# Performance work log

Measured on AMD Instinct MI355X. Metric: run time of the kernel, lower is better.

Reference implementation:

```python
import jax, jax.numpy as jnp
import numpy as np

BANDS, D_MODEL, NCLASS = 200, 256, 17
EXPAND, D_STATE, D_CONV, HEADDIM = 2, 128, 4, 64
D_INNER = EXPAND * D_MODEL            # 512
NHEADS = D_INNER // HEADDIM           # 8
D_IN_PROJ = 2 * D_INNER + 2 * D_STATE + NHEADS  # 1288 (ngroups=1)
CHUNK = 256


def _segsum(a):
    # a: (..., Q) -> (..., Q, Q); out[i,j] = sum_{k=j+1..i} a[k] (i>=j), else -inf
    q = a.shape[-1]
    cs = jnp.cumsum(a, axis=-1)
    d = cs[..., :, None] - cs[..., None, :]
    mask = jnp.tril(jnp.ones((q, q), dtype=bool))
    return jnp.where(mask, d, -jnp.inf)


def _ssd(Xd, Adt, B, C, Q):
    # Chunked SSD (exact selective-scan). Xd=(b,l,h,p) is x*dt, Adt=(b,l,h) is A*dt, B,C=(b,l,n)
    b, l, h, p = Xd.shape
    n = B.shape[-1]
    c = l // Q
    Xc = Xd.reshape(b, c, Q, h, p)
    Bc = B.reshape(b, c, Q, n)
    Cc = C.reshape(b, c, Q, n)
    Ac = Adt.reshape(b, c, Q, h).transpose(0, 3, 1, 2)      # (b,h,c,Q)
    Acs = jnp.cumsum(Ac, axis=-1)
    Lm = jnp.exp(_segsum(Ac))                                # (b,h,c,Q,Q) lower-tri decay
    Yd = jnp.einsum('bcqn,bckn,bhcqk,bckhp->bcqhp', Cc, Bc, Lm, Xc)
    decay_states = jnp.exp(Acs[..., -1:] - Acs)              # (b,h,c,Q)
    states = jnp.einsum('bcqn,bhcq,bcqhp->bchpn', Bc, decay_states, Xc)
    chunk_decay = jnp.exp(Acs[..., -1])                      # (b,h,c)
    def step(carry, inp):
        s, d = inp
        return carry * d[..., None, None] + s, carry
    _, prev = jax.lax.scan(step, jnp.zeros((b, h, p, n), Xd.dtype),
                           (states.transpose(1, 0, 2, 3, 4), chunk_decay.transpose(2, 0, 1)))
    prev = prev.transpose(1, 0, 2, 3, 4)                     # (b,c,h,p,n) state entering each chunk
    Yo = jnp.einsum('bcqn,bchpn,bhcq->bcqhp', Cc, prev, jnp.exp(Acs))
    return (Yd + Yo).reshape(b, l, h, p)


def setup_inputs() -> dict:
    ks = jax.random.split(jax.random.key(0), 8)
    b, l = 16, 1024
    dt0 = jnp.exp(jax.random.uniform(ks[1], (NHEADS,), minval=np.log(1e-3), maxval=np.log(0.1)))
    return {
        'x': jax.random.normal(ks[0], (b, l, BANDS), jnp.float32),
        'w_inp': jax.random.normal(ks[2], (BANDS, D_MODEL)) * 0.05,
        'b_inp': jnp.zeros((D_MODEL,)),
        'w_in': jax.random.normal(ks[3], (D_MODEL, D_IN_PROJ)) * 0.05,
        'conv_w': jax.random.normal(ks[4], (D_CONV, D_INNER + 2 * D_STATE)) * 0.2,
        'conv_b': jnp.zeros((D_INNER + 2 * D_STATE,)),
        'dt_bias': jnp.log(jnp.expm1(dt0)),                 # inverse softplus
        'A_log': jnp.log(jnp.arange(1, NHEADS + 1, dtype=jnp.float32)),
        'D': jnp.ones((NHEADS,)),
        'rms_w': jnp.ones((D_INNER,)),
        'w_out': jax.random.normal(ks[5], (D_INNER, D_MODEL)) * 0.04,
        'ln_g': jnp.ones((D_MODEL,)),
        'ln_b': jnp.zeros((D_MODEL,)),
        'w_cls': jax.random.normal(ks[6], (D_MODEL, NCLASS)) * 0.06,
        'b_cls': jnp.zeros((NCLASS,)),
    }


def reference(x, w_inp, b_inp, w_in, conv_w, conv_b, dt_bias, A_log, D,
              rms_w, w_out, ln_g, ln_b, w_cls, b_cls):
    b, l, _ = x.shape
    u = x @ w_inp + b_inp                                    # input_proj: (b,l,d_model)
    zxbcdt = u @ w_in                                        # (b,l,1288)
    z, xBC, dt = jnp.split(zxbcdt, [D_INNER, 2 * D_INNER + 2 * D_STATE], axis=-1)
    dt = jax.nn.softplus(dt + dt_bias)                       # (b,l,nheads)
    # causal depthwise conv1d + SiLU
    xBC = jax.lax.conv_general_dilated(
        xBC, conv_w[:, None, :], (1,), [(D_CONV - 1, 0)],
        dimension_numbers=('NWC', 'WIO', 'NWC'),
        feature_group_count=D_INNER + 2 * D_STATE) + conv_b
    xBC = jax.nn.silu(xBC)
    xh, B, C = jnp.split(xBC, [D_INNER, D_INNER + D_STATE], axis=-1)
    xh = xh.reshape(b, l, NHEADS, HEADDIM)
    A = -jnp.exp(A_log)                                      # (nheads,)
    y = _ssd(xh * dt[..., None], dt * A, B, C, CHUNK)        # (b,l,h,p)
    y = y + xh * D[None, None, :, None]                      # D skip
    y = y.reshape(b, l, D_INNER)
    # gated RMSNorm (norm_before_gate=False): rmsnorm(y * silu(z)) * w
    y = y * jax.nn.silu(z)
    y = y * jax.lax.rsqrt(jnp.mean(y * y, axis=-1, keepdims=True) + 1e-5) * rms_w
    y = y @ w_out                                            # out_proj (no bias)
    # classifier: LayerNorm -> Dropout(eval=identity) -> Linear
    mu = jnp.mean(y, axis=-1, keepdims=True)
    var = jnp.mean((y - mu) ** 2, axis=-1, keepdims=True)
    y = (y - mu) * jax.lax.rsqrt(var + 1e-5) * ln_g + ln_b
    return y @ w_cls + b_cls
```

## Files before the change

kernel.cpp:

```cpp
#include <hip/hip_runtime.h>
#include <math.h>

#define ROWS   16384L
#define LSEQ   1024
#define NB     16
#define DM     256
#define DPROJ  1288
#define ZXW    1280
#define XBCW   768
#define DIN    512
#define DSTATE 128
#define NH     8
#define HD     64
#define QLEN   256
#define NCHUNK 4
#define NCLS   17

typedef __attribute__((ext_vector_type(8))) short s16x8;
typedef __attribute__((ext_vector_type(8))) unsigned short u16x8;
typedef __attribute__((ext_vector_type(4))) float f32x4;

#define GLOAD_LDS16(gsrc, ldst) \
  __builtin_amdgcn_global_load_lds((const __attribute__((address_space(1))) void*)(gsrc), \
      (__attribute__((address_space(3))) void*)(ldst), 16, 0, 0)

constexpr long O_GBF  = 0;
constexpr long O_ZX   = O_GBF + ROWS*DM;
constexpr long O_XBC  = O_ZX  + ROWS*DPROJ;
constexpr long O_DT   = O_XBC + ROWS*XBCW;
constexpr long O_ACS  = O_DT  + ROWS*NH;
constexpr long O_Y    = O_ACS + 131072;
constexpr long O_ST   = O_Y   + ROWS*DIN;
constexpr long O_Y2   = O_ST  + 4194304;
constexpr long O_XBF  = O_XBC;
constexpr long O_BBF  = O_XBC + 4200000;
constexpr long O_CBF  = O_XBC + 5300000;
constexpr long O_BT   = O_XBC + 6400000;
constexpr long O_YBF  = O_Y;
constexpr long O_XPBF = O_Y + 4300000;
constexpr long O_WCT  = O_Y + 6200000;
constexpr long O_WOUTT= O_Y + 6400000;
constexpr long O_WDT  = O_Y + 6500000;
constexpr long O_WCLST= O_Y + 6530000;
constexpr long O_WINT = O_Y + 6600000;
constexpr long O_WIPE = O_Y + 6800000;

__device__ inline unsigned short f2bf(float f) {
  union { float f; unsigned u; } v; v.f = f;
  unsigned r = v.u + 0x7FFFu + ((v.u >> 16) & 1u);
  return (unsigned short)(r >> 16);
}
__device__ inline float bf2f(unsigned short s) {
  union { unsigned u; float f; } v; v.u = ((unsigned)s) << 16; return v.f;
}

__device__ inline void xcd_swizzle(int gx, int& bx, int& by) {
  int nwg = gx * (int)gridDim.y;
  int lid = (int)blockIdx.y * gx + (int)blockIdx.x;
  int q = nwg >> 3, r = nwg & 7;
  int xcd = lid & 7, idx = lid >> 3;
  int base = xcd < r ? xcd * (q + 1) : r * (q + 1) + (xcd - r) * q;
  int w = base + idx;
  bx = w % gx; by = w / gx;
}

__global__ __launch_bounds__(256) void prep_misc(
    const float* __restrict__ x, unsigned short* __restrict__ xp,
    const float* __restrict__ w_in, unsigned short* __restrict__ w_inT,
    const float* __restrict__ wout, unsigned short* __restrict__ woutT,
    const float* __restrict__ w_inp, const float* __restrict__ b_inp,
    unsigned short* __restrict__ we,
    float* __restrict__ Wdt, float* __restrict__ bdt,
    const float* __restrict__ wcls, float* __restrict__ wclsT)
{
  int bid = blockIdx.x;
  int tid = threadIdx.x;
  if (bid < 3584) {
    long idx = (long)bid * 256 + tid;
    int q = (int)(idx % 56);
    long row = idx / 56;
    ushort4 o = {0, 0, 0, 0};
    if (q < 50) {
      float4 v = *(const float4*)&x[row * 200 + q * 4];
      o.x = f2bf(v.x); o.y = f2bf(v.y); o.z = f2bf(v.z); o.w = f2bf(v.w);
    } else if (q == 50) {
      o.x = 0x3F80;
    }
    *(ushort4*)&xp[row * 224 + q * 4] = o;
  } else if (bid < 4872) {
    long i = (long)(bid - 3584) * 256 + tid;
    int k = (int)(i & 255);
    long n = i >> 8;
    w_inT[i] = f2bf(w_in[(long)k * DPROJ + n]);
  } else if (bid < 5384) {
    long i = (long)(bid - 4872) * 256 + tid;
    int k = (int)(i & 511);
    long n = i >> 9;
    woutT[i] = f2bf(wout[(long)k * DM + n]);
  } else if (bid < 5608) {
    int i = (bid - 5384) * 256 + tid;
    int k = i >> 8, j = i & 255;
    float v = 0.f;
    if (k < 200)       v = w_inp[(long)k * 256 + j];
    else if (k == 200) v = b_inp[j];
    we[i] = f2bf(v);
  } else if (bid < 5659) {
    int k = (bid - 5608) * 4 + (tid >> 6);
    if (k > 200) return;
    int lane = tid & 63;
    int j0 = lane * 4;
    float4 xv = (k < 200) ? *(const float4*)&w_inp[(long)k * 256 + j0]
                          : *(const float4*)&b_inp[j0];
    float a0 = 0.f, a1 = 0.f, a2 = 0.f, a3 = 0.f, a4 = 0.f, a5 = 0.f, a6 = 0.f, a7 = 0.f;
    float xd[4] = {xv.x, xv.y, xv.z, xv.w};
#pragma unroll
    for (int d = 0; d < 4; ++d) {
      const float* wr = &w_in[(long)(j0 + d) * DPROJ + 1280];
      float4 wa = *(const float4*)wr;
      float4 wb = *(const float4*)(wr + 4);
      a0 = fmaf(xd[d], wa.x, a0); a1 = fmaf(xd[d], wa.y, a1);
      a2 = fmaf(xd[d], wa.z, a2); a3 = fmaf(xd[d], wa.w, a3);
      a4 = fmaf(xd[d], wb.x, a4); a5 = fmaf(xd[d], wb.y, a5);
      a6 = fmaf(xd[d], wb.z, a6); a7 = fmaf(xd[d], wb.w, a7);
    }
#pragma unroll
    for (int off = 32; off; off >>= 1) {
      a0 += __shfl_xor(a0, off); a1 += __shfl_xor(a1, off);
      a2 += __shfl_xor(a2, off); a3 += __shfl_xor(a3, off);
      a4 += __shfl_xor(a4, off); a5 += __shfl_xor(a5, off);
      a6 += __shfl_xor(a6, off); a7 += __shfl_xor(a7, off);
    }
    float o = a0;
    if (lane == 1) o = a1; if (lane == 2) o = a2; if (lane == 3) o = a3;
    if (lane == 4) o = a4; if (lane == 5) o = a5; if (lane == 6) o = a6;
    if (lane == 7) o = a7;
    if (lane < 8) {
      if (k < 200) Wdt[k * 8 + lane] = o;
      else         bdt[lane] = o;
    }
  } else {
    int i = (bid - 5659) * 256 + tid;
    if (i < NCLS * 256) {
      int j = i >> 8, k = i & 255;
      wclsT[i] = wcls[(long)k * NCLS + j];
    }
  }
}

__global__ __launch_bounds__(256) void gemm_bf16(
    const unsigned short* __restrict__ A, const unsigned short* __restrict__ BT,
    float* __restrict__ C, unsigned short* __restrict__ Cb,
    const float* __restrict__ bias, int M, int N, int K)
{
  int bx, by;
  xcd_swizzle(gridDim.x, bx, by);
  __shared__ __align__(16) unsigned short As[128 * 32];
  __shared__ __align__(16) unsigned short Bs[128 * 32];
  const int tid = threadIdx.x;
  const int m0 = by * 128, n0 = bx * 128;
  const int lane = tid & 63, wv = tid >> 6;
  const int wr = (wv >> 1) * 64, wc = (wv & 1) * 64;
  f32x4 acc[4][4];
#pragma unroll
  for (int i = 0; i < 4; ++i)
#pragma unroll
    for (int j = 0; j < 4; ++j) acc[i][j] = (f32x4){0.f, 0.f, 0.f, 0.f};

  for (int k0 = 0; k0 < K; k0 += 32) {
    __syncthreads();
#pragma unroll
    for (int s = 0; s < 2; ++s) {
      int idx = (tid + 256 * s) * 8;
      int r = idx >> 5, kk = idx & 31;
      GLOAD_LDS16(&A[(long)(m0 + r) * K + k0 + kk], &As[idx]);
    }
#pragma unroll
    for (int s = 0; s < 2; ++s) {
      int idx = (tid + 256 * s) * 8;
      int n = idx >> 5, kk = idx & 31;
      int srcn = (n0 + n < N) ? (n0 + n) : 0;
      GLOAD_LDS16(&BT[(long)srcn * K + k0 + kk], &Bs[idx]);
    }
    __syncthreads();
    s16x8 af[4], bf[4];
#pragma unroll
    for (int i = 0; i < 4; ++i)
      af[i] = *(const s16x8*)&As[(wr + i * 16 + (lane & 15)) * 32 + (lane >> 4) * 8];
#pragma unroll
    for (int j = 0; j < 4; ++j)
      bf[j] = *(const s16x8*)&Bs[(wc + j * 16 + (lane & 15)) * 32 + (lane >> 4) * 8];
    __builtin_amdgcn_s_setprio(1);
#pragma unroll
    for (int i = 0; i < 4; ++i)
#pragma unroll
      for (int j = 0; j < 4; ++j)
        acc[i][j] = __builtin_amdgcn_mfma_f32_16x16x32_bf16(af[i], bf[j], acc[i][j], 0, 0, 0);
    __builtin_amdgcn_s_setprio(0);
  }
  const int cr = (lane >> 4) * 4, cc = lane & 15;
#pragma unroll
  for (int i = 0; i < 4; ++i)
#pragma unroll
    for (int j = 0; j < 4; ++j) {
      int col = n0 + wc + j * 16 + cc;
      if (col < N) {
        long rowb = (long)(m0 + wr + i * 16 + cr);
        float bv = bias ? bias[col] : 0.f;
#pragma unroll
        for (int r = 0; r < 4; ++r) {
          float v = acc[i][j][r] + bv;
          if (C)  C[(rowb + r) * N + col] = v;
          if (Cb) Cb[(rowb + r) * (long)N + col] = f2bf(v);
        }
      }
    }
}

__global__ __launch_bounds__(256) void trans_g(
    const unsigned short* __restrict__ Bbf, unsigned short* __restrict__ BbfT,
    const unsigned short* __restrict__ Cbf, unsigned short* __restrict__ Gbf)
{
  const int bid = blockIdx.x;
  const int tid = threadIdx.x;
  if (bid < 128) {
    __shared__ unsigned short T[128][130];
    int bc = bid >> 1, kh = bid & 1;
    long rowbase = (long)(bc >> 2) * LSEQ + (bc & 3) * QLEN + kh * 128;
    for (int e = tid; e < 128 * 128; e += 256) {
      int r = e >> 7, n = e & 127;
      T[r][n] = Bbf[(rowbase + r) * 128 + n];
    }
    __syncthreads();
    for (int e = tid; e < 128 * 128; e += 256) {
      int n = e >> 7, k = e & 127;
      BbfT[((long)bc * 128 + n) * 256 + kh * 128 + k] = T[k][n];
    }
    return;
  }
  if (bid >= 320) {
    int bc = bid - 320;
    unsigned short* Gout = Gbf + (long)bc * 65536;
    s16x8 z = {};
    for (int e = tid; e < 128 * 16; e += 256) {
      int r = e >> 4, seg = e & 15;
      *(s16x8*)&Gout[(long)r * 256 + 128 + seg * 8] = z;
    }
    return;
  }
  int bid2 = bid - 128;
  int t = bid2 % 3, bc = bid2 / 3;
  int m0 = (t == 0) ? 0 : 128;
  int n0 = (t == 2) ? 128 : 0;
  unsigned short* Gout = Gbf + (long)bc * 65536;
  long rowbase = (long)(bc >> 2) * LSEQ + (bc & 3) * QLEN;
  const unsigned short* A  = Cbf + rowbase * 128;
  const unsigned short* BT = Bbf + rowbase * 128;
  __shared__ __align__(16) unsigned short As[128 * 32];
  __shared__ __align__(16) unsigned short Bs[128 * 32];
  const int lane = tid & 63, wv = tid >> 6;
  const int wr = (wv >> 1) * 64, wc = (wv & 1) * 64;
  f32x4 acc[4][4];
#pragma unroll
  for (int i = 0; i < 4; ++i)
#pragma unroll
    for (int j = 0; j < 4; ++j) acc[i][j] = (f32x4){0.f, 0.f, 0.f, 0.f};
  for (int k0 = 0; k0 < 128; k0 += 32) {
    __syncthreads();
#pragma unroll
    for (int s = 0; s < 2; ++s) {
      int idx = (tid + 256 * s) * 8;
      int r = idx >> 5, kk = idx & 31;
      GLOAD_LDS16(&A[(long)(m0 + r) * 128 + k0 + kk], &As[idx]);
      GLOAD_LDS16(&BT[(long)(n0 + r) * 128 + k0 + kk], &Bs[idx]);
    }
    __syncthreads();
    s16x8 af[4], bf[4];
#pragma unroll
    for (int i = 0; i < 4; ++i)
      af[i] = *(const s16x8*)&As[(wr + i * 16 + (lane & 15)) * 32 + (lane >> 4) * 8];
#pragma unroll
    for (int j = 0; j < 4; ++j)
      bf[j] = *(const s16x8*)&Bs[(wc + j * 16 + (lane & 15)) * 32 + (lane >> 4) * 8];
    __builtin_amdgcn_s_setprio(1);
#pragma unroll
    for (int i = 0; i < 4; ++i)
#pragma unroll
      for (int j = 0; j < 4; ++j)
        acc[i][j] = __builtin_amdgcn_mfma_f32_16x16x32_bf16(af[i], bf[j], acc[i][j], 0, 0, 0);
    __builtin_amdgcn_s_setprio(0);
  }
  const int cr = (lane >> 4) * 4, cc = lane & 15;
#pragma unroll
  for (int i = 0; i < 4; ++i)
#pragma unroll
    for (int j = 0; j < 4; ++j) {
      int col = n0 + wc + j * 16 + cc;
      int qb = m0 + wr + i * 16 + cr;
#pragma unroll
      for (int r = 0; r < 4; ++r)
        Gout[(long)(qb + r) * 256 + col] = (col <= qb + r) ? f2bf(acc[i][j][r]) : (unsigned short)0;
    }
}

__global__ __launch_bounds__(256) void conv_silu5(
    const unsigned short* __restrict__ zxb, const float* __restrict__ cw,
    const float* __restrict__ cb,
    unsigned short* __restrict__ Xbf, unsigned short* __restrict__ Bbf,
    unsigned short* __restrict__ Cbf)
{
  long idx = (long)blockIdx.x * 256 + threadIdx.x;
  if (idx >= (ROWS / 4) * 96) return;
  int co = (int)(idx % 96);
  long tmp = idx / 96;
  int tq = (int)(tmp & 255);
  int b = (int)(tmp >> 8);
  int ch = co * 8;
  long row0 = (long)b * LSEQ + tq * 4;
  u16x8 zv[7];
#pragma unroll
  for (int j = 0; j < 7; ++j) {
    if (j >= 3 || tq > 0)
      zv[j] = *(const u16x8*)&zxb[(row0 + j - 3) * ZXW + 512 + ch];
    else
      zv[j] = (u16x8){0, 0, 0, 0, 0, 0, 0, 0};
  }
  float cwv[4][8], cbv[8];
  {
    float4 b0 = *(const float4*)&cb[ch];
    float4 b1 = *(const float4*)&cb[ch + 4];
    cbv[0] = b0.x; cbv[1] = b0.y; cbv[2] = b0.z; cbv[3] = b0.w;
    cbv[4] = b1.x; cbv[5] = b1.y; cbv[6] = b1.z; cbv[7] = b1.w;
  }
#pragma unroll
  for (int w = 0; w < 4; ++w) {
    float4 c0 = *(const float4*)&cw[w * XBCW + ch];
    float4 c1 = *(const float4*)&cw[w * XBCW + ch + 4];
    cwv[w][0] = c0.x; cwv[w][1] = c0.y; cwv[w][2] = c0.z; cwv[w][3] = c0.w;
    cwv[w][4] = c1.x; cwv[w][5] = c1.y; cwv[w][6] = c1.z; cwv[w][7] = c1.w;
  }
#pragma unroll
  for (int i = 0; i < 4; ++i) {
    float a[8];
#pragma unroll
    for (int k = 0; k < 8; ++k) a[k] = cbv[k];
#pragma unroll
    for (int w = 0; w < 4; ++w) {
#pragma unroll
      for (int k = 0; k < 8; ++k)
        a[k] = fmaf(bf2f(zv[i + w][k]), cwv[w][k], a[k]);
    }
    u16x8 o;
#pragma unroll
    for (int k = 0; k < 8; ++k)
      o[k] = f2bf(a[k] / (1.f + __expf(-a[k])));
    long row = row0 + i;
    if (ch < 512)      *(u16x8*)&Xbf[row * DIN + ch] = o;
    else if (ch < 640) *(u16x8*)&Bbf[row * 128 + ch - 512] = o;
    else               *(u16x8*)&Cbf[row * 128 + ch - 640] = o;
  }
}

__global__ __launch_bounds__(256) void dt_logits(
    const float* __restrict__ x, const float* __restrict__ Wdt,
    const float* __restrict__ bdt, const float* __restrict__ dtb,
    float* __restrict__ dtsp)
{
  __shared__ float xs[32][201];
  __shared__ float wdt_s[1600];
  long row0 = (long)blockIdx.x * 32;
  int tid = threadIdx.x;
#pragma unroll
  for (int s = 0; s < 25; ++s) {
    int e = tid + s * 256;
    int r = e / 200, c = e % 200;
    xs[r][c] = x[(row0 + r) * 200 + c];
  }
#pragma unroll
  for (int s = 0; s < 7; ++s) {
    int e = tid + s * 256;
    if (e < 1600) wdt_s[e] = Wdt[e];
  }
  __syncthreads();
  int r = tid >> 3, h = tid & 7;
  float acc = dtb[h] + bdt[h];
  for (int i = 0; i < 200; ++i)
    acc = fmaf(xs[r][i], wdt_s[i * 8 + h], acc);
  float sp = (acc > 20.f) ? acc : log1pf(__expf(acc));
  dtsp[(row0 + r) * NH + h] = sp;
}

__global__ __launch_bounds__(256) void dt_cumsum4(
    const float* __restrict__ dtsp, const float* __restrict__ alog,
    float* __restrict__ acs)
{
  int g = ((int)blockIdx.x * 256 + (int)threadIdx.x) >> 6;
  int lane = threadIdx.x & 63;
  int c = g & 3, h = (g >> 2) & 7, b = g >> 5;
  float Ah = -__expf(alog[h]);
  long rowbase = (long)b * LSEQ + c * QLEN;
  long abase = (((long)b * NH + h) * NCHUNK + c) * QLEN;
  float v[4];
#pragma unroll
  for (int j = 0; j < 4; ++j)
    v[j] = dtsp[(rowbase + lane * 4 + j) * NH + h] * Ah;
  v[1] += v[0]; v[2] += v[1]; v[3] += v[2];
  float tot = v[3];
  float run = tot;
#pragma unroll
  for (int d = 1; d < 64; d <<= 1) {
    float t = __shfl_up(run, d);
    if (lane >= d) run += t;
  }
  float excl = run - tot;
#pragma unroll
  for (int j = 0; j < 4; ++j) acs[abase + lane * 4 + j] = excl + v[j];
}

__global__ __launch_bounds__(256) void yd_states7(
    const unsigned short* __restrict__ Xbf, const float* __restrict__ dtsp,
    const float* __restrict__ acs, const unsigned short* __restrict__ Gbf,
    const unsigned short* __restrict__ BbfT,
    unsigned short* __restrict__ ybf, unsigned short* __restrict__ st)
{
  int bid = blockIdx.x;
  int xcd = bid & 7, i0 = bid >> 3;
  int bc = xcd * 8 + (i0 >> 4);
  int rem = i0 & 15, h = rem >> 1, half = rem & 1;
  int c = bc & 3, b = bc >> 2;
  int bch = bc * 8 + h;

  __shared__ __align__(16) unsigned short XdT[64][264];
  __shared__ float AcsS[256], E1f[256], E2f[256], dts[256];

  const int tid = threadIdx.x;
  const int lane = tid & 63, wv = tid >> 6;
  const bool ydw = wv < 2;
  const int qb = half == 0 ? (wv == 0 ? 0 : 3) : (wv == 0 ? 1 : 2);
  const int q0 = qb * 64;
  const int n0w = half * 64 + (wv - 2) * 32;
  long rowbase = (long)b * LSEQ + c * QLEN;
  const unsigned short* Gb  = Gbf + (long)bc * 65536;
  const unsigned short* BTg = BbfT + (long)bc * 32768;

  AcsS[tid] = acs[(((long)b * NH + h) * NCHUNK + c) * QLEN + tid];
  dts[tid]  = dtsp[(rowbase + tid) * NH + h];
  __syncthreads();
  E1f[tid] = __expf(AcsS[tid] - AcsS[tid | 63]);
  E2f[tid] = __expf(AcsS[tid | 63] - AcsS[tid]);
  float rs_[4];
  rs_[0] = 1.f;
#pragma unroll
  for (int kt = 1; kt < 4; ++kt) rs_[kt] = __expf(AcsS[kt * 64 + 63] - AcsS[kt * 64 - 1]);
  __syncthreads();
  {
    int kb = wv * 64;
#pragma unroll
    for (int s = 0; s < 16; ++s) {
      int k4 = kb + s * 4;
      ushort4 pk;
      unsigned short* pp = (unsigned short*)&pk;
#pragma unroll
      for (int j = 0; j < 4; ++j) {
        int k = k4 + j;
        float v = bf2f(Xbf[(rowbase + k) * DIN + h * HD + lane]) * dts[k] * E2f[k];
        pp[j] = f2bf(v);
      }
      *(ushort4*)&XdT[lane][k4] = pk;
    }
  }
  __syncthreads();

  f32x4 accY[4][4], accS[4][2];
#pragma unroll
  for (int i = 0; i < 4; ++i)
#pragma unroll
    for (int j = 0; j < 4; ++j) accY[i][j] = (f32x4){0.f, 0.f, 0.f, 0.f};
#pragma unroll
  for (int i = 0; i < 4; ++i)
#pragma unroll
    for (int j = 0; j < 2; ++j) accS[i][j] = (f32x4){0.f, 0.f, 0.f, 0.f};

  for (int kt = 0; kt < 4; ++kt) {
    int qlo = kt * 64;
    if (ydw) {
      if (qb >= kt) {
        if (kt)
#pragma unroll
          for (int i = 0; i < 4; ++i)
#pragma unroll
            for (int j = 0; j < 4; ++j) accY[i][j] *= rs_[kt];
#pragma unroll
        for (int ks = 0; ks < 2; ++ks) {
          s16x8 bfr[4];
#pragma unroll
          for (int j = 0; j < 4; ++j)
            bfr[j] = *(const s16x8*)&XdT[j * 16 + (lane & 15)][qlo + ks * 32 + (lane >> 4) * 8];
          __builtin_amdgcn_s_setprio(1);
#pragma unroll
          for (int i = 0; i < 4; ++i) {
            s16x8 a = *(const s16x8*)&Gb[(long)(q0 + i * 16 + (lane & 15)) * 256 + qlo + ks * 32 + (lane >> 4) * 8];
#pragma unroll
            for (int j = 0; j < 4; ++j)
              accY[i][j] = __builtin_amdgcn_mfma_f32_16x16x32_bf16(a, bfr[j], accY[i][j], 0, 0, 0);
          }
          __builtin_amdgcn_s_setprio(0);
        }
      }
    } else {
      if (kt)
#pragma unroll
        for (int i = 0; i < 4; ++i)
#pragma unroll
          for (int j = 0; j < 2; ++j) accS[i][j] *= rs_[kt];
#pragma unroll
      for (int ks = 0; ks < 2; ++ks) {
        s16x8 afx[4];
#pragma unroll
        for (int i = 0; i < 4; ++i)
          afx[i] = *(const s16x8*)&XdT[i * 16 + (lane & 15)][qlo + ks * 32 + (lane >> 4) * 8];
        __builtin_amdgcn_s_setprio(1);
#pragma unroll
        for (int j2 = 0; j2 < 2; ++j2) {
          s16x8 bt = *(const s16x8*)&BTg[(long)(n0w + j2 * 16 + (lane & 15)) * 256 + qlo + ks * 32 + (lane >> 4) * 8];
#pragma unroll
          for (int i = 0; i < 4; ++i)
            accS[i][j2] = __builtin_amdgcn_mfma_f32_16x16x32_bf16(afx[i], bt, accS[i][j2], 0, 0, 0);
        }
        __builtin_amdgcn_s_setprio(0);
      }
    }
  }
  const int cr = (lane >> 4) * 4, cc = lane & 15;
  if (ydw) {
#pragma unroll
    for (int i = 0; i < 4; ++i)
#pragma unroll
      for (int j = 0; j < 4; ++j) {
        int q = q0 + i * 16 + cr;
        int p = j * 16 + cc;
#pragma unroll
        for (int r = 0; r < 4; ++r)
          ybf[(rowbase + q + r) * DIN + h * HD + p] = f2bf(accY[i][j][r] * E1f[q + r]);
      }
  } else {
#pragma unroll
    for (int i = 0; i < 4; ++i)
#pragma unroll
      for (int j2 = 0; j2 < 2; ++j2) {
        int p = i * 16 + cr;
        int n = n0w + j2 * 16 + cc;
#pragma unroll
        for (int r = 0; r < 4; ++r)
          st[(long)bch * 8192 + (long)(p + r) * 128 + n] = f2bf(accS[i][j2][r]);
      }
  }
}

__global__ void scan_states(unsigned short* __restrict__ st, const float* __restrict__ acs)
{
  long idx = (long)blockIdx.x * 256 + threadIdx.x;
  if (idx >= (long)NB * NH * 2048) return;
  long inner = idx & 2047;
  int h = (int)((idx >> 11) & 7);
  int b = (int)(idx >> 14);
  f32x4 carry = {0.f, 0.f, 0.f, 0.f};
  for (int c = 0; c < NCHUNK; ++c) {
    float dc = __expf(acs[(((long)b * NH + h) * NCHUNK + c) * QLEN + (QLEN - 1)]);
    long si = (((long)(b * NCHUNK + c) * NH + h) << 13) + inner * 4;
    ushort4 s4 = *(ushort4*)&st[si];
    f32x4 s = {bf2f(s4.x), bf2f(s4.y), bf2f(s4.z), bf2f(s4.w)};
    ushort4 o = {f2bf(carry[0]), f2bf(carry[1]), f2bf(carry[2]), f2bf(carry[3])};
    *(ushort4*)&st[si] = o;
    carry = carry * dc + s;
  }
}

__global__ __launch_bounds__(256) void yo_combine6(
    const unsigned short* __restrict__ Xbf, const unsigned short* __restrict__ Cbf,
    const unsigned short* __restrict__ prev, const float* __restrict__ acs,
    const float* __restrict__ Dp, unsigned short* __restrict__ ybf)
{
  int bid = blockIdx.x;
  int xcd = bid & 7, i0 = bid >> 3;
  int bc = xcd * 8 + (i0 >> 3), h = i0 & 7;
  int c = bc & 3, b = bc >> 2;
  int bch = bc * 8 + h;
  __shared__ float EqA[QLEN];
  const int tid = threadIdx.x;
  const int lane = tid & 63, wv = tid >> 6;
  long rowbase = (long)b * LSEQ + c * QLEN;
  EqA[tid] = __expf(acs[(((long)b * NH + h) * NCHUNK + c) * QLEN + tid]);
  __syncthreads();
  const unsigned short* Cb = Cbf + rowbase * 128;
  const unsigned short* pv = prev + (long)bch * 8192;
  f32x4 acc[4][4];
#pragma unroll
  for (int i = 0; i < 4; ++i)
#pragma unroll
    for (int j = 0; j < 4; ++j) acc[i][j] = (f32x4){0.f, 0.f, 0.f, 0.f};
#pragma unroll
  for (int ks = 0; ks < 4; ++ks) {
    int n0 = ks * 32 + (lane >> 4) * 8;
    s16x8 bf[4];
#pragma unroll
    for (int j = 0; j < 4; ++j) {
      int p = j * 16 + (lane & 15);
      bf[j] = *(const s16x8*)&pv[p * 128 + n0];
    }
    __builtin_amdgcn_s_setprio(1);
#pragma unroll
    for (int i = 0; i < 4; ++i) {
      s16x8 af = *(const s16x8*)&Cb[(long)(wv * 64 + i * 16 + (lane & 15)) * 128 + n0];
#pragma unroll
      for (int j = 0; j < 4; ++j)
        acc[i][j] = __builtin_amdgcn_mfma_f32_16x16x32_bf16(af, bf[j], acc[i][j], 0, 0, 0);
    }
    __builtin_amdgcn_s_setprio(0);
  }
  const int cr = (lane >> 4) * 4, cc = lane & 15;
  float Dh = Dp[h];
#pragma unroll
  for (int i = 0; i < 4; ++i)
#pragma unroll
    for (int j = 0; j < 4; ++j) {
      int q = wv * 64 + i * 16 + cr;
      int p = j * 16 + cc;
#pragma unroll
      for (int r = 0; r < 4; ++r) {
        long row = rowbase + q + r;
        long yi = row * DIN + h * HD + p;
        float xh = bf2f(Xbf[yi]);
        float pr = bf2f(ybf[yi]);
        ybf[yi] = f2bf(pr + acc[i][j][r] * EqA[q + r] + xh * Dh);
      }
    }
}

__global__ __launch_bounds__(256) void gated_rms4(
    unsigned short* __restrict__ ybf, const unsigned short* __restrict__ zxb,
    const float* __restrict__ rmsw)
{
  long row = (long)blockIdx.x * 4 + (threadIdx.x >> 6);
  int lane = threadIdx.x & 63;
  u16x8 yv = *(const u16x8*)&ybf[row * DIN + lane * 8];
  u16x8 zv = *(const u16x8*)&zxb[row * ZXW + lane * 8];
  float v[8];
  float ss = 0.f;
#pragma unroll
  for (int i = 0; i < 8; ++i) {
    float z = bf2f(zv[i]);
    v[i] = bf2f(yv[i]) * (z / (1.f + __expf(-z)));
    ss = fmaf(v[i], v[i], ss);
  }
#pragma unroll
  for (int off = 32; off; off >>= 1) ss += __shfl_xor(ss, off);
  float scale = rsqrtf(ss * (1.f / DIN) + 1e-5f);
  u16x8 o;
#pragma unroll
  for (int i = 0; i < 8; ++i) {
    float w = rmsw[lane * 8 + i];
    o[i] = f2bf(v[i] * scale * w);
  }
  *(u16x8*)&ybf[row * DIN + lane * 8] = o;
}

__global__ __launch_bounds__(256) void ln_cls2(
    const unsigned short* __restrict__ y2b, const float* __restrict__ g,
    const float* __restrict__ bb, const float* __restrict__ wclsT,
    const float* __restrict__ bcls, float* __restrict__ out)
{
  long row = (long)blockIdx.x * 4 + (threadIdx.x >> 6);
  int lane = threadIdx.x & 63;
  ushort4 yv = *(const ushort4*)&y2b[row * DM + lane * 4];
  float v0 = bf2f(yv.x), v1 = bf2f(yv.y), v2 = bf2f(yv.z), v3 = bf2f(yv.w);
  float s = v0 + v1 + v2 + v3;
  float q = v0 * v0 + v1 * v1 + v2 * v2 + v3 * v3;
#pragma unroll
  for (int off = 32; off; off >>= 1) {
    s += __shfl_xor(s, off);
    q += __shfl_xor(q, off);
  }
  float mu = s * (1.f / DM);
  float rstd = rsqrtf(q * (1.f / DM) - mu * mu + 1e-5f);
  float4 gv = *(const float4*)&g[lane * 4];
  float4 bv = *(const float4*)&bb[lane * 4];
  float y0 = (v0 - mu) * rstd * gv.x + bv.x;
  float y1 = (v1 - mu) * rstd * gv.y + bv.y;
  float y2_ = (v2 - mu) * rstd * gv.z + bv.z;
  float y3 = (v3 - mu) * rstd * gv.w + bv.w;
  float accs[NCLS];
#pragma unroll
  for (int j = 0; j < NCLS; ++j) {
    float4 wv = *(const float4*)&wclsT[j * 256 + lane * 4];
    accs[j] = y0 * wv.x + y1 * wv.y + y2_ * wv.z + y3 * wv.w;
  }
#pragma unroll
  for (int off = 32; off; off >>= 1)
#pragma unroll
    for (int j = 0; j < NCLS; ++j) accs[j] += __shfl_xor(accs[j], off);
  float o = accs[0] + bcls[0];
#pragma unroll
  for (int j = 1; j < NCLS; ++j)
    if (lane == j) o = accs[j] + bcls[j];
  if (lane < NCLS) out[row * NCLS + lane] = o;
}

extern "C" void kernel_launch(void* const* d_in, const int* in_sizes, int n_in,
                              void* d_out, int out_size, void* d_ws, size_t ws_size,
                              hipStream_t stream)
{
  const float* x     = (const float*)d_in[0];
  const float* w_inp = (const float*)d_in[1];
  const float* b_inp = (const float*)d_in[2];
  const float* w_in  = (const float*)d_in[3];
  const float* convw = (const float*)d_in[4];
  const float* convb = (const float*)d_in[5];
  const float* dtb   = (const float*)d_in[6];
  const float* alog  = (const float*)d_in[7];
  const float* Dp    = (const float*)d_in[8];
  const float* rmsw  = (const float*)d_in[9];
  const float* wout  = (const float*)d_in[10];
  const float* lng   = (const float*)d_in[11];
  const float* lnb   = (const float*)d_in[12];
  const float* wcls  = (const float*)d_in[13];
  const float* bcls  = (const float*)d_in[14];
  float* out = (float*)d_out;
  float* ws  = (float*)d_ws;

  float* dtsp = ws + O_DT;
  float* acs  = ws + O_ACS;
  float* Wdt  = ws + O_WDT;
  float* bdt  = Wdt + 1600;
  float* wclsT= ws + O_WCLST;
  unsigned short* Gbf    = (unsigned short*)(ws + O_GBF);
  unsigned short* zxb    = (unsigned short*)(ws + O_ZX);
  unsigned short* Xbf    = (unsigned short*)(ws + O_XBF);
  unsigned short* Bbf    = (unsigned short*)(ws + O_BBF);
  unsigned short* Cbf    = (unsigned short*)(ws + O_CBF);
  unsigned short* BbfT   = (unsigned short*)(ws + O_BT);
  unsigned short* ybf    = (unsigned short*)(ws + O_YBF);
  unsigned short* xp_bf  = (unsigned short*)(ws + O_XPBF);
  unsigned short* WcombT = (unsigned short*)(ws + O_WCT);
  unsigned short* woutT  = (unsigned short*)(ws + O_WOUTT);
  unsigned short* w_inT  = (unsigned short*)(ws + O_WINT);
  unsigned short* we_bf  = (unsigned short*)(ws + O_WIPE);
  unsigned short* st     = (unsigned short*)(ws + O_ST);
  unsigned short* y2b    = (unsigned short*)(ws + O_Y2);

  prep_misc<<<5676, 256, 0, stream>>>(x, xp_bf, w_in, w_inT, wout, woutT,
                                      w_inp, b_inp, we_bf, Wdt, bdt, wcls, wclsT);
  gemm_bf16<<<dim3(2, 11), 256, 0, stream>>>(w_inT, we_bf, nullptr, WcombT, nullptr, 1408, 224, 256);
  gemm_bf16<<<dim3(10, 128), 256, 0, stream>>>(xp_bf, WcombT, nullptr, zxb, nullptr, 16384, ZXW, 224);
  conv_silu5<<<1536, 256, 0, stream>>>(zxb, convw, convb, Xbf, Bbf, Cbf);
  dt_logits<<<512, 256, 0, stream>>>(x, Wdt, bdt, dtb, dtsp);
  dt_cumsum4<<<128, 256, 0, stream>>>(dtsp, alog, acs);
  trans_g<<<384, 256, 0, stream>>>(Bbf, BbfT, Cbf, Gbf);
  yd_states7<<<1024, 256, 0, stream>>>(Xbf, dtsp, acs, Gbf, BbfT, ybf, st);
  scan_states<<<1024, 256, 0, stream>>>(st, acs);
  yo_combine6<<<512, 256, 0, stream>>>(Xbf, Cbf, st, acs, Dp, ybf);
  gated_rms4<<<4096, 256, 0, stream>>>(ybf, zxb, rmsw);
  gemm_bf16<<<dim3(2, 128), 256, 0, stream>>>(ybf, woutT, nullptr, y2b, nullptr, 16384, DM, DIN);
  ln_cls2<<<4096, 256, 0, stream>>>(y2b, lng, lnb, wclsT, bcls, out);
}
```

Baseline: 184.4 us.

## Fuse inter-chunk state scan into Yo combine kernel

Removes the separate scan_states kernel and instead has each Yo block rebuild its incoming state from the raw per-chunk states, weighting earlier chunks by exponentials of the accumulated chunk-end decays. Chunk 0 now skips the Yo matmul entirely. This saves one kernel launch and a read-modify-write pass over the state buffer, at the cost of redundant state loads and FMA work in blocks for later chunks. Rounding also changes slightly, because the combined state is formed in fp32 and rounded to bf16 once.

```diff
diff --git a/kernel.cpp b/kernel.cpp
--- a/kernel.cpp
+++ b/kernel.cpp
@@ -556,66 +556,72 @@
   }
 }
 
-__global__ void scan_states(unsigned short* __restrict__ st, const float* __restrict__ acs)
-{
-  long idx = (long)blockIdx.x * 256 + threadIdx.x;
-  if (idx >= (long)NB * NH * 2048) return;
-  long inner = idx & 2047;
-  int h = (int)((idx >> 11) & 7);
-  int b = (int)(idx >> 14);
-  f32x4 carry = {0.f, 0.f, 0.f, 0.f};
-  for (int c = 0; c < NCHUNK; ++c) {
-    float dc = __expf(acs[(((long)b * NH + h) * NCHUNK + c) * QLEN + (QLEN - 1)]);
-    long si = (((long)(b * NCHUNK + c) * NH + h) << 13) + inner * 4;
-    ushort4 s4 = *(ushort4*)&st[si];
-    f32x4 s = {bf2f(s4.x), bf2f(s4.y), bf2f(s4.z), bf2f(s4.w)};
-    ushort4 o = {f2bf(carry[0]), f2bf(carry[1]), f2bf(carry[2]), f2bf(carry[3])};
-    *(ushort4*)&st[si] = o;
-    carry = carry * dc + s;
-  }
-}
-
-__global__ __launch_bounds__(256) void yo_combine6(
+__global__ __launch_bounds__(256) void yo_combine7(
     const unsigned short* __restrict__ Xbf, const unsigned short* __restrict__ Cbf,
-    const unsigned short* __restrict__ prev, const float* __restrict__ acs,
+    const unsigned short* __restrict__ st, const float* __restrict__ acs,
     const float* __restrict__ Dp, unsigned short* __restrict__ ybf)
 {
   int bid = blockIdx.x;
   int xcd = bid & 7, i0 = bid >> 3;
   int bc = xcd * 8 + (i0 >> 3), h = i0 & 7;
   int c = bc & 3, b = bc >> 2;
-  int bch = bc * 8 + h;
   __shared__ float EqA[QLEN];
   const int tid = threadIdx.x;
   const int lane = tid & 63, wv = tid >> 6;
   long rowbase = (long)b * LSEQ + c * QLEN;
-  EqA[tid] = __expf(acs[(((long)b * NH + h) * NCHUNK + c) * QLEN + tid]);
+  long abase = ((long)b * NH + h) * NCHUNK;
+  EqA[tid] = __expf(acs[(abase + c) * QLEN + tid]);
   __syncthreads();
   const unsigned short* Cb = Cbf + rowbase * 128;
-  const unsigned short* pv = prev + (long)bch * 8192;
+  const long sb0 = ((long)(b * 4 + 0) * 8 + h) * 8192;
+  const long sb1 = ((long)(b * 4 + 1) * 8 + h) * 8192;
+  const long sb2 = ((long)(b * 4 + 2) * 8 + h) * 8192;
+  float aend1 = (c >= 2) ? acs[(abase + 1) * QLEN + (QLEN - 1)] : 0.f;
+  float aend2 = (c >= 3) ? acs[(abase + 2) * QLEN + (QLEN - 1)] : 0.f;
+  float w0 = (c == 2) ? __expf(aend1) : ((c == 3) ? __expf(aend1 + aend2) : 1.f);
+  float w1 = (c == 3) ? __expf(aend2) : 1.f;
+
   f32x4 acc[4][4];
 #pragma unroll
   for (int i = 0; i < 4; ++i)
 #pragma unroll
     for (int j = 0; j < 4; ++j) acc[i][j] = (f32x4){0.f, 0.f, 0.f, 0.f};
-#pragma unroll
-  for (int ks = 0; ks < 4; ++ks) {
-    int n0 = ks * 32 + (lane >> 4) * 8;
-    s16x8 bf[4];
-#pragma unroll
-    for (int j = 0; j < 4; ++j) {
-      int p = j * 16 + (lane & 15);
-      bf[j] = *(const s16x8*)&pv[p * 128 + n0];
-    }
-    __builtin_amdgcn_s_setprio(1);
-#pragma unroll
-    for (int i = 0; i < 4; ++i) {
-      s16x8 af = *(const s16x8*)&Cb[(long)(wv * 64 + i * 16 + (lane & 15)) * 128 + n0];
-#pragma unroll
-      for (int j = 0; j < 4; ++j)
-        acc[i][j] = __builtin_amdgcn_mfma_f32_16x16x32_bf16(af, bf[j], acc[i][j], 0, 0, 0);
-    }
-    __builtin_amdgcn_s_setprio(0);
+  if (c > 0) {
+#pragma unroll
+    for (int ks = 0; ks < 4; ++ks) {
+      int n0 = ks * 32 + (lane >> 4) * 8;
+      s16x8 bf[4];
+#pragma unroll
+      for (int j = 0; j < 4; ++j) {
+        int p = j * 16 + (lane & 15);
+        long off = (long)p * 128 + n0;
+        if (c == 1) {
+          bf[j] = *(const s16x8*)&st[sb0 + off];
+        } else if (c == 2) {
+          u16x8 s0 = *(const u16x8*)&st[sb0 + off];
+          u16x8 s1 = *(const u16x8*)&st[sb1 + off];
+#pragma unroll
+          for (int k = 0; k < 8; ++k)
+            bf[j][k] = (short)f2bf(fmaf(bf2f(s0[k]), w0, bf2f(s1[k])));
+        } else {
+          u16x8 s0 = *(const u16x8*)&st[sb0 + off];
+          u16x8 s1 = *(const u16x8*)&st[sb1 + off];
+          u16x8 s2 = *(const u16x8*)&st[sb2 + off];
+#pragma unroll
+          for (int k = 0; k < 8; ++k)
+            bf[j][k] = (short)f2bf(fmaf(bf2f(s0[k]), w0, fmaf(bf2f(s1[k]), w1, bf2f(s2[k]))));
+        }
+      }
+      __builtin_amdgcn_s_setprio(1);
+#pragma unroll
+      for (int i = 0; i < 4; ++i) {
+        s16x8 af = *(const s16x8*)&Cb[(long)(wv * 64 + i * 16 + (lane & 15)) * 128 + n0];
+#pragma unroll
+        for (int j = 0; j < 4; ++j)
+          acc[i][j] = __builtin_amdgcn_mfma_f32_16x16x32_bf16(af, bf[j], acc[i][j], 0, 0, 0);
+      }
+      __builtin_amdgcn_s_setprio(0);
+    }
   }
   const int cr = (lane >> 4) * 4, cc = lane & 15;
   float Dh = Dp[h];
@@ -756,8 +762,7 @@
   dt_cumsum4<<<128, 256, 0, stream>>>(dtsp, alog, acs);
   trans_g<<<384, 256, 0, stream>>>(Bbf, BbfT, Cbf, Gbf);
   yd_states7<<<1024, 256, 0, stream>>>(Xbf, dtsp, acs, Gbf, BbfT, ybf, st);
-  scan_states<<<1024, 256, 0, stream>>>(st, acs);
-  yo_combine6<<<512, 256, 0, stream>>>(Xbf, Cbf, st, acs, Dp, ybf);
+  yo_combine7<<<512, 256, 0, stream>>>(Xbf, Cbf, st, acs, Dp, ybf);
   gated_rms4<<<4096, 256, 0, stream>>>(ybf, zxb, rmsw);
   gemm_bf16<<<dim3(2, 128), 256, 0, stream>>>(ybf, woutT, nullptr, y2b, nullptr, 16384, DM, DIN);
   ln_cls2<<<4096, 256, 0, stream>>>(y2b, lng, lnb, wclsT, bcls, out);
```

Result: slower. 188.2 us (+2.1%).
